# Optimization experiments

Hardware: AMD Instinct MI355X
Metric: run time of the kernel (lower is better)

Reference implementation:

```python
import jax, jax.numpy as jnp
import numpy as np

N_NODES = 25000
N_EDGES = 400000
EMBED_DIM = 128
NUM_HEADS = 8
D_K = EMBED_DIM // NUM_HEADS


def setup_inputs() -> dict:
    key = jax.random.key(0)
    ks = jax.random.split(key, 8)
    sc = 1.0 / np.sqrt(EMBED_DIM)
    return {
        "x": jax.random.normal(ks[0], (N_NODES, EMBED_DIM), jnp.float32),
        "edge_index": jax.random.randint(ks[1], (2, N_EDGES), 0, N_NODES),
        "attn_bias": jax.random.normal(ks[2], (N_EDGES, NUM_HEADS), jnp.float32),
        "Wq": jax.random.normal(ks[3], (EMBED_DIM, EMBED_DIM), jnp.float32) * sc,
        "bq": jnp.zeros((EMBED_DIM,), jnp.float32),
        "Wk": jax.random.normal(ks[4], (EMBED_DIM, EMBED_DIM), jnp.float32) * sc,
        "bk": jnp.zeros((EMBED_DIM,), jnp.float32),
        "Wv": jax.random.normal(ks[5], (EMBED_DIM, EMBED_DIM), jnp.float32) * sc,
        "bv": jnp.zeros((EMBED_DIM,), jnp.float32),
        "Wo": jax.random.normal(ks[6], (EMBED_DIM, EMBED_DIM), jnp.float32) * sc,
        "bo": jnp.zeros((EMBED_DIM,), jnp.float32),
    }


def reference(x, edge_index, attn_bias, Wq, bq, Wk, bk, Wv, bv, Wo, bo):
    N = x.shape[0]
    E = edge_index.shape[1]
    H, dk = NUM_HEADS, D_K
    scale = 1.0 / np.sqrt(dk).astype(np.float32)
    dst = edge_index[0]  # query/aggregation node per edge
    src = edge_index[1]  # key/value node per edge

    # project at node level (as torch: linear(x)[index]), then gather per edge
    q = (x @ Wq.T + bq)[dst].reshape(E, H, dk)
    k = (x @ Wk.T + bk)[src].reshape(E, H, dk)
    v = (x @ Wv.T + bv)[src].reshape(E, H, dk)

    logits = scale * jnp.sum(q * k, axis=2) + attn_bias  # [E, H]

    # segment softmax over edges grouped by destination node
    m = jax.ops.segment_max(logits, dst, num_segments=N)     # [N, H]
    e = jnp.exp(logits - m[dst])                              # [E, H]
    z = jax.ops.segment_sum(e, dst, num_segments=N)           # [N, H]
    scores = e / z[dst]                                       # [E, H]

    agg = jax.ops.segment_sum(scores[..., None] * v, dst, num_segments=N)  # [N, H, dk]
    out = agg.reshape(N, H * dk) @ Wo.T + bo                   # [N, embed_dim]
    return out, logits[..., None]
```

## Files before the change

### kernel.cpp

```cpp
#include <hip/hip_runtime.h>
#include <math.h>

#define N_NODES 25000
#define N_EDGES 400000
#define EMBED   128
#define HEADS   8
#define DK      16
#define MAXDEG  96
#define NX (N_NODES * 128)
#define GBLK 391
#define SCAT_BLK 391

typedef __attribute__((ext_vector_type(8))) short bf16x8;
typedef __attribute__((ext_vector_type(4))) float f32x4;
typedef unsigned int uint;
typedef unsigned short ushort;

__device__ inline uint pack2_bf16(float a, float b) {
    union { float f; uint u; } ua, ub;
    ua.f = a; ub.f = b;
    uint ra = (ua.u + 0x7FFFu + ((ua.u >> 16) & 1u)) >> 16;
    uint rb = (ub.u + 0x7FFFu + ((ub.u >> 16) & 1u)) >> 16;
    return (ra & 0xFFFFu) | (rb << 16);
}
__device__ inline ushort cvt_bf16(float a) {
    union { float f; uint u; } ua; ua.f = a;
    return (ushort)((ua.u + 0x7FFFu + ((ua.u >> 16) & 1u)) >> 16);
}
__device__ inline float bf16_lo(uint u) {
    union { uint u; float f; } x; x.u = u << 16; return x.f;
}
__device__ inline float bf16_hi(uint u) {
    union { uint u; float f; } x; x.u = u & 0xFFFF0000u; return x.f;
}

__global__ __launch_bounds__(256) void prep(
    const float* __restrict__ Wq, const float* __restrict__ Wk,
    const float* __restrict__ Wv, const float* __restrict__ Wo,
    ushort* __restrict__ wb, int* __restrict__ deg)
{
    int i = blockIdx.x * 256 + threadIdx.x;
    if (i < N_NODES) deg[i] = 0;
    if (i < 32768) {
        int j = i * 2;
        const float* src = (j < 16384) ? Wq + j
                         : (j < 32768) ? Wk + (j - 16384)
                         : (j < 49152) ? Wv + (j - 32768)
                         :               Wo + (j - 49152);
        float2 v = *reinterpret_cast<const float2*>(src);
        reinterpret_cast<uint*>(wb)[i] = pack2_bf16(v.x, v.y);
    }
}

__global__ __launch_bounds__(256) void gemm_qkv_scatter(
    const float* __restrict__ x, const ushort* __restrict__ Wall,
    const float* __restrict__ bq, const float* __restrict__ bk,
    const float* __restrict__ bv,
    ushort* __restrict__ Qb, ushort* __restrict__ Kb, ushort* __restrict__ Vb,
    const int* __restrict__ ei, int* __restrict__ deg, int2* __restrict__ csr2)
{
    const int bx = blockIdx.x;
    if (bx >= 3 * GBLK) {
        int t = (bx - 3 * GBLK) * 256 + threadIdx.x;
        int e = t * 4;
        if (e < N_EDGES) {
            int4 d = *reinterpret_cast<const int4*>(ei + e);
            int4 s = *reinterpret_cast<const int4*>(ei + N_EDGES + e);
            int p0 = atomicAdd(&deg[d.x], 1);
            if (p0 < MAXDEG) csr2[d.x * MAXDEG + p0] = make_int2(e, s.x);
            int p1 = atomicAdd(&deg[d.y], 1);
            if (p1 < MAXDEG) csr2[d.y * MAXDEG + p1] = make_int2(e + 1, s.y);
            int p2 = atomicAdd(&deg[d.z], 1);
            if (p2 < MAXDEG) csr2[d.z * MAXDEG + p2] = make_int2(e + 2, s.z);
            int p3 = atomicAdd(&deg[d.w], 1);
            if (p3 < MAXDEG) csr2[d.w * MAXDEG + p3] = make_int2(e + 3, s.w);
        }
        return;
    }

    const int which = bx / GBLK;
    const int mb    = bx - which * GBLK;
    const ushort* W = Wall + which * 16384;
    const float* bias = (which == 0) ? bq : (which == 1) ? bk : bv;
    ushort* C = (which == 0) ? Qb : (which == 1) ? Kb : Vb;

    const int lane = threadIdx.x & 63;
    const int wave = threadIdx.x >> 6;
    const int ml   = lane & 15;
    const int quad = lane >> 4;
    const int m0   = mb * 64 + wave * 16;

    int arow = m0 + ml; if (arow >= N_NODES) arow = N_NODES - 1;
    const float* xp = x + arow * 128 + quad * 8;

    bf16x8 af[4];
#pragma unroll
    for (int ks = 0; ks < 4; ++ks) {
        float4 a0 = *reinterpret_cast<const float4*>(xp + ks * 32);
        float4 a1 = *reinterpret_cast<const float4*>(xp + ks * 32 + 4);
        uint* u = reinterpret_cast<uint*>(&af[ks]);
        u[0] = pack2_bf16(a0.x, a0.y); u[1] = pack2_bf16(a0.z, a0.w);
        u[2] = pack2_bf16(a1.x, a1.y); u[3] = pack2_bf16(a1.z, a1.w);
    }

    f32x4 acc[8];
#pragma unroll
    for (int ct = 0; ct < 8; ++ct) acc[ct] = (f32x4){0.f, 0.f, 0.f, 0.f};

#pragma unroll
    for (int ks = 0; ks < 4; ++ks) {
#pragma unroll
        for (int ct = 0; ct < 8; ++ct) {
            bf16x8 bf = *reinterpret_cast<const bf16x8*>(
                W + (ct * 16 + ml) * 128 + ks * 32 + quad * 8);
            acc[ct] = __builtin_amdgcn_mfma_f32_16x16x32_bf16(af[ks], bf, acc[ct], 0, 0, 0);
        }
    }

#pragma unroll
    for (int ct = 0; ct < 8; ++ct) {
        int col = ct * 16 + ml;
        float b = bias[col];
#pragma unroll
        for (int r = 0; r < 4; ++r) {
            int row = m0 + quad * 4 + r;
            if (row < N_NODES)
                C[row * 128 + col] = cvt_bf16(acc[ct][r] + b);
        }
    }
}

__global__ __launch_bounds__(256) void gemm_out(
    const ushort* __restrict__ A, const ushort* __restrict__ W,
    const float* __restrict__ bias, float* __restrict__ C, int M)
{
    const int lane = threadIdx.x & 63;
    const int wave = threadIdx.x >> 6;
    const int ml   = lane & 15;
    const int quad = lane >> 4;
    const int m0   = blockIdx.x * 64 + wave * 16;
    const int ct0  = blockIdx.y * 4;

    int arow = m0 + ml; if (arow >= M) arow = M - 1;
    const ushort* ap = A + arow * 128 + quad * 8;

    f32x4 acc[4];
#pragma unroll
    for (int ct = 0; ct < 4; ++ct) acc[ct] = (f32x4){0.f, 0.f, 0.f, 0.f};

#pragma unroll
    for (int ks = 0; ks < 128; ks += 32) {
        bf16x8 af = *reinterpret_cast<const bf16x8*>(ap + ks);
#pragma unroll
        for (int ct = 0; ct < 4; ++ct) {
            bf16x8 bf = *reinterpret_cast<const bf16x8*>(
                W + ((ct0 + ct) * 16 + ml) * 128 + ks + quad * 8);
            acc[ct] = __builtin_amdgcn_mfma_f32_16x16x32_bf16(af, bf, acc[ct], 0, 0, 0);
        }
    }

#pragma unroll
    for (int ct = 0; ct < 4; ++ct) {
        int col = (ct0 + ct) * 16 + ml;
        float bv_ = bias[col];
#pragma unroll
        for (int r = 0; r < 4; ++r) {
            int row = m0 + quad * 4 + r;
            if (row < M)
                C[row * 128 + col] = acc[ct][r] + bv_;
        }
    }
}

__global__ __launch_bounds__(256) void fused_attn(
    const ushort* __restrict__ Q2, const ushort* __restrict__ K2,
    const ushort* __restrict__ V2,
    const float* __restrict__ attn_bias,
    const int* __restrict__ deg, const int2* __restrict__ csr2,
    float* __restrict__ logits, ushort* __restrict__ AGG)
{
    const int lane = threadIdx.x & 63;
    const int wid  = threadIdx.x >> 6;
    const int n = blockIdx.x * 4 + wid;
    int dg = deg[n]; if (dg > MAXDEG) dg = MAXDEG;
    const int start = n * MAXDEG;
    const int h  = lane & 7;
    const int es = lane >> 3;

    const uint4* Qu4 = reinterpret_cast<const uint4*>(Q2);
    const uint4* Ku4 = reinterpret_cast<const uint4*>(K2);
    const uint4* Vu4 = reinterpret_cast<const uint4*>(V2);

    uint4 qa = Qu4[n * 16 + h * 2];
    uint4 qb = Qu4[n * 16 + h * 2 + 1];
    float qf[16];
    {
        uint qq[8] = {qa.x, qa.y, qa.z, qa.w, qb.x, qb.y, qb.z, qb.w};
#pragma unroll
        for (int j = 0; j < 8; ++j) {
            qf[2 * j]     = bf16_lo(qq[j]);
            qf[2 * j + 1] = bf16_hi(qq[j]);
        }
    }

    float acc[16];
#pragma unroll
    for (int j = 0; j < 16; ++j) acc[j] = 0.f;
    float z = 0.f;

    if (dg > 0) {
        int2 ep = csr2[start + (es < dg ? es : dg - 1)];
        for (int base = 0; base < dg; base += 8) {
            int e = ep.x, s = ep.y;
            bool valid = (base + es) < dg;

            uint4 k0 = Ku4[s * 16 + h * 2];
            uint4 k1 = Ku4[s * 16 + h * 2 + 1];
            uint4 v0 = Vu4[s * 16 + h * 2];
            uint4 v1 = Vu4[s * 16 + h * 2 + 1];
            float bias = attn_bias[e * 8 + h];

            int nb = base + 8;
            if (nb < dg) {
                int t2 = nb + es; if (t2 >= dg) t2 = dg - 1;
                ep = csr2[start + t2];
            }

            uint kk[8] = {k0.x, k0.y, k0.z, k0.w, k1.x, k1.y, k1.z, k1.w};
            float d = 0.f;
#pragma unroll
            for (int j = 0; j < 8; ++j)
                d += qf[2 * j] * bf16_lo(kk[j]) + qf[2 * j + 1] * bf16_hi(kk[j]);

            float l = 0.25f * d + bias;
            float p = 0.f;
            if (valid) {
                __builtin_nontemporal_store(l, &logits[e * 8 + h]);
                p = __expf(l);
            }
            z += p;

            uint vv[8] = {v0.x, v0.y, v0.z, v0.w, v1.x, v1.y, v1.z, v1.w};
#pragma unroll
            for (int j = 0; j < 8; ++j) {
                acc[2 * j]     += p * bf16_lo(vv[j]);
                acc[2 * j + 1] += p * bf16_hi(vv[j]);
            }
        }
    }

    {
        int bit = (lane >> 5) & 1;
#pragma unroll
        for (int j = 0; j < 8; ++j) {
            float send = bit ? acc[j] : acc[j + 8];
            float keep = bit ? acc[j + 8] : acc[j];
            acc[j] = keep + __shfl_xor(send, 32, 64);
        }
        bit = (lane >> 4) & 1;
#pragma unroll
        for (int j = 0; j < 4; ++j) {
            float send = bit ? acc[j] : acc[j + 4];
            float keep = bit ? acc[j + 4] : acc[j];
            acc[j] = keep + __shfl_xor(send, 16, 64);
        }
        bit = (lane >> 3) & 1;
#pragma unroll
        for (int j = 0; j < 2; ++j) {
            float send = bit ? acc[j] : acc[j + 2];
            float keep = bit ? acc[j + 2] : acc[j];
            acc[j] = keep + __shfl_xor(send, 8, 64);
        }
    }
    z += __shfl_xor(z, 8, 64);
    z += __shfl_xor(z, 16, 64);
    z += __shfl_xor(z, 32, 64);

    float inv = (z > 0.f) ? 1.f / z : 0.f;
    int d_off = ((lane >> 5) & 1) * 8 + ((lane >> 4) & 1) * 4 + ((lane >> 3) & 1) * 2;
    reinterpret_cast<uint*>(AGG)[n * 64 + h * 8 + (d_off >> 1)] =
        pack2_bf16(acc[0] * inv, acc[1] * inv);
}

extern "C" void kernel_launch(void* const* d_in, const int* in_sizes, int n_in,
                              void* d_out, int out_size, void* d_ws, size_t ws_size,
                              hipStream_t stream)
{
    const float* x         = (const float*)d_in[0];
    const int*   ei        = (const int*)  d_in[1];
    const float* attn_bias = (const float*)d_in[2];
    const float* Wq = (const float*)d_in[3];
    const float* bq = (const float*)d_in[4];
    const float* Wk = (const float*)d_in[5];
    const float* bk = (const float*)d_in[6];
    const float* Wv = (const float*)d_in[7];
    const float* bv = (const float*)d_in[8];
    const float* Wo = (const float*)d_in[9];
    const float* bo = (const float*)d_in[10];

    float* out    = (float*)d_out;
    float* logits = out + N_NODES * EMBED;

    ushort* wb   = (ushort*)d_ws;
    ushort* Qb   = wb + 4 * 16384;
    ushort* Kb   = Qb + NX;
    ushort* Vb   = Kb + NX;
    ushort* AGGb = Vb + NX;
    int* deg     = (int*)(AGGb + NX);
    int2* csr2   = (int2*)(deg + N_NODES);

    prep<<<128, 256, 0, stream>>>(Wq, Wk, Wv, Wo, wb, deg);

    gemm_qkv_scatter<<<3 * GBLK + SCAT_BLK, 256, 0, stream>>>(
        x, wb, bq, bk, bv, Qb, Kb, Vb, ei, deg, csr2);

    fused_attn<<<N_NODES / 4, 256, 0, stream>>>(Qb, Kb, Vb, attn_bias,
                                                deg, csr2, logits, AGGb);

    gemm_out<<<dim3(GBLK, 2), 256, 0, stream>>>(AGGb, wb + 3 * 16384, bo,
                                                out, N_NODES);
}
```

Baseline: 188.6 us.

## Fuse output projection into attention kernel via shared-memory MFMA tile

The attention kernel now writes each node's aggregated bf16 vector into a padded shared-memory tile, and after a block barrier one wave multiplies the 4 real rows (zero-padded to 16) by Wo using MFMA and writes the final output with bias. This removes the separate output GEMM launch and the global round trip of the AGG buffer. In exchange, each block reloads all of Wo from cache, 12 of the 16 MFMA rows are padding, and the other three waves sit idle during the projection.

```diff
diff --git a/kernel.cpp b/kernel.cpp
--- a/kernel.cpp
+++ b/kernel.cpp
@@ -130,62 +130,31 @@
     }
 }
 
-__global__ __launch_bounds__(256) void gemm_out(
-    const ushort* __restrict__ A, const ushort* __restrict__ W,
-    const float* __restrict__ bias, float* __restrict__ C, int M)
-{
-    const int lane = threadIdx.x & 63;
-    const int wave = threadIdx.x >> 6;
-    const int ml   = lane & 15;
-    const int quad = lane >> 4;
-    const int m0   = blockIdx.x * 64 + wave * 16;
-    const int ct0  = blockIdx.y * 4;
-
-    int arow = m0 + ml; if (arow >= M) arow = M - 1;
-    const ushort* ap = A + arow * 128 + quad * 8;
-
-    f32x4 acc[4];
-#pragma unroll
-    for (int ct = 0; ct < 4; ++ct) acc[ct] = (f32x4){0.f, 0.f, 0.f, 0.f};
-
-#pragma unroll
-    for (int ks = 0; ks < 128; ks += 32) {
-        bf16x8 af = *reinterpret_cast<const bf16x8*>(ap + ks);
-#pragma unroll
-        for (int ct = 0; ct < 4; ++ct) {
-            bf16x8 bf = *reinterpret_cast<const bf16x8*>(
-                W + ((ct0 + ct) * 16 + ml) * 128 + ks + quad * 8);
-            acc[ct] = __builtin_amdgcn_mfma_f32_16x16x32_bf16(af, bf, acc[ct], 0, 0, 0);
-        }
-    }
-
-#pragma unroll
-    for (int ct = 0; ct < 4; ++ct) {
-        int col = (ct0 + ct) * 16 + ml;
-        float bv_ = bias[col];
-#pragma unroll
-        for (int r = 0; r < 4; ++r) {
-            int row = m0 + quad * 4 + r;
-            if (row < M)
-                C[row * 128 + col] = acc[ct][r] + bv_;
-        }
-    }
-}
-
-__global__ __launch_bounds__(256) void fused_attn(
+__global__ __launch_bounds__(256) void fused_attn_out(
     const ushort* __restrict__ Q2, const ushort* __restrict__ K2,
     const ushort* __restrict__ V2,
     const float* __restrict__ attn_bias,
     const int* __restrict__ deg, const int2* __restrict__ csr2,
-    float* __restrict__ logits, ushort* __restrict__ AGG)
+    const ushort* __restrict__ Wo2, const float* __restrict__ bo,
+    float* __restrict__ logits, float* __restrict__ out)
 {
-    const int lane = threadIdx.x & 63;
-    const int wid  = threadIdx.x >> 6;
-    const int n = blockIdx.x * 4 + wid;
+    __shared__ ushort agg_sh[16 * 136];
+
+    const int tid  = threadIdx.x;
+    const int lane = tid & 63;
+    const int wid  = tid >> 6;
+    const int n0 = blockIdx.x * 4;
+    const int n  = n0 + wid;
     int dg = deg[n]; if (dg > MAXDEG) dg = MAXDEG;
     const int start = n * MAXDEG;
     const int h  = lane & 7;
     const int es = lane >> 3;
+    const int ml   = lane & 15;
+    const int quad = lane >> 4;
+
+    if (tid < 204)
+        *reinterpret_cast<uint4*>(reinterpret_cast<char*>(agg_sh) + 1088 + tid * 16) =
+            make_uint4(0u, 0u, 0u, 0u);
 
     const uint4* Qu4 = reinterpret_cast<const uint4*>(Q2);
     const uint4* Ku4 = reinterpret_cast<const uint4*>(K2);
@@ -278,8 +247,44 @@
 
     float inv = (z > 0.f) ? 1.f / z : 0.f;
     int d_off = ((lane >> 5) & 1) * 8 + ((lane >> 4) & 1) * 4 + ((lane >> 3) & 1) * 2;
-    reinterpret_cast<uint*>(AGG)[n * 64 + h * 8 + (d_off >> 1)] =
+    *reinterpret_cast<uint*>(reinterpret_cast<char*>(agg_sh) + wid * 272 +
+                             (h * 16 + d_off) * 2) =
         pack2_bf16(acc[0] * inv, acc[1] * inv);
+
+    __syncthreads();
+
+    if (wid == 0) {
+        bf16x8 af[4];
+#pragma unroll
+        for (int ks = 0; ks < 4; ++ks)
+            af[ks] = *reinterpret_cast<const bf16x8*>(
+                reinterpret_cast<char*>(agg_sh) + ml * 272 + ks * 64 + quad * 16);
+
+        f32x4 oacc[8];
+#pragma unroll
+        for (int ct = 0; ct < 8; ++ct) oacc[ct] = (f32x4){0.f, 0.f, 0.f, 0.f};
+
+#pragma unroll
+        for (int ks = 0; ks < 4; ++ks) {
+#pragma unroll
+            for (int ct = 0; ct < 8; ++ct) {
+                bf16x8 bf = *reinterpret_cast<const bf16x8*>(
+                    Wo2 + (ct * 16 + ml) * 128 + ks * 32 + quad * 8);
+                oacc[ct] = __builtin_amdgcn_mfma_f32_16x16x32_bf16(af[ks], bf, oacc[ct], 0, 0, 0);
+            }
+        }
+
+        if (quad == 0) {
+#pragma unroll
+            for (int ct = 0; ct < 8; ++ct) {
+                int col = ct * 16 + ml;
+                float b = bo[col];
+#pragma unroll
+                for (int r = 0; r < 4; ++r)
+                    out[(n0 + r) * 128 + col] = oacc[ct][r] + b;
+            }
+        }
+    }
 }
 
 extern "C" void kernel_launch(void* const* d_in, const int* in_sizes, int n_in,
@@ -305,8 +310,7 @@
     ushort* Qb   = wb + 4 * 16384;
     ushort* Kb   = Qb + NX;
     ushort* Vb   = Kb + NX;
-    ushort* AGGb = Vb + NX;
-    int* deg     = (int*)(AGGb + NX);
+    int* deg     = (int*)(Vb + NX);
     int2* csr2   = (int2*)(deg + N_NODES);
 
     prep<<<128, 256, 0, stream>>>(Wq, Wk, Wv, Wo, wb, deg);
@@ -314,9 +318,7 @@
     gemm_qkv_scatter<<<3 * GBLK + SCAT_BLK, 256, 0, stream>>>(
         x, wb, bq, bk, bv, Qb, Kb, Vb, ei, deg, csr2);
 
-    fused_attn<<<N_NODES / 4, 256, 0, stream>>>(Qb, Kb, Vb, attn_bias,
-                                                deg, csr2, logits, AGGb);
-
-    gemm_out<<<dim3(GBLK, 2), 256, 0, stream>>>(AGGb, wb + 3 * 16384, bo,
-                                                out, N_NODES);
-}
+    fused_attn_out<<<N_NODES / 4, 256, 0, stream>>>(Qb, Kb, Vb, attn_bias,
+                                                    deg, csr2, wb + 3 * 16384,
+                                                    bo, logits, out);
+}
```

After: 185.8 us. Within noise of the previous version (-1.5%).
